# Performance work log

Hardware: AMD Instinct MI355X
Metric: run time of the kernel (lower is better)

The kernel has to match this reference:

```python
import jax, jax.numpy as jnp
import numpy as np

GROUPSIZE = 128

def _unpack_int4(packed, axis):
    # packed: int32 array; unpack 8 nibbles per int32 along `axis`.
    shifts = (jnp.arange(8, dtype=jnp.int32) * 4)
    expanded = jnp.expand_dims(packed, axis + 1)  # [..., P, 1, ...]
    shp = [1] * expanded.ndim
    shp[axis + 1] = 8
    nib = (expanded >> shifts.reshape(shp)) & 0xF
    new_shape = list(packed.shape)
    new_shape[axis] = packed.shape[axis] * 8
    return nib.reshape(new_shape)

def setup_inputs() -> dict:
    key = jax.random.key(0)
    k1, k2, k3, k4, k5 = jax.random.split(key, 5)
    in_f, out_f = 4096, 4096
    n_tokens = 8192
    n_groups = in_f // GROUPSIZE
    x = jax.random.normal(k1, (n_tokens, in_f), dtype=jnp.float32)
    qweight = jax.random.randint(k2, (in_f // 8, out_f), 0, 2147483647, dtype=jnp.int32)
    qzeros = jax.random.randint(k3, (n_groups, out_f // 8), 0, 2147483647, dtype=jnp.int32)
    scales = jax.random.uniform(k4, (n_groups, out_f), dtype=jnp.float32) * 0.01
    g_idx = (jnp.arange(in_f, dtype=jnp.int32) // GROUPSIZE).astype(jnp.int32)
    bias = jax.random.normal(k5, (out_f,), dtype=jnp.float32) * 0.01
    return {"x": x, "qweight": qweight, "qzeros": qzeros,
            "scales": scales, "g_idx": g_idx, "bias": bias}

def reference(x, qweight, qzeros, scales, g_idx, bias):
    # Dequantize int4 GPTQ weights: W[k,n] = scales[g_idx[k],n] * (wq[k,n] - (zq[g_idx[k],n]+1))
    wq = _unpack_int4(qweight, axis=0)          # [in, out] int32 nibbles
    zq = _unpack_int4(qzeros, axis=1) + 1       # [n_groups, out]
    scale_k = scales[g_idx]                     # [in, out]
    zero_k = zq[g_idx]                          # [in, out]
    w = scale_k * (wq.astype(x.dtype) - zero_k.astype(x.dtype))  # [in, out]
    return x @ w + bias
```

## Files before the change

kernel.cpp:

```cpp
#include <hip/hip_runtime.h>

typedef __attribute__((ext_vector_type(4))) float  f32x4;
typedef __attribute__((ext_vector_type(8))) short  short8;
typedef __attribute__((ext_vector_type(4))) short  short4v;

#define M_TOK 8192
#define N_OUT 4096
#define K_IN  4096
#define NT    64

typedef const __attribute__((address_space(1))) void* gp_t;
typedef __attribute__((address_space(3))) void* lp_t;
__device__ __forceinline__ void gl_lds16(const void* g, void* l) {
    __builtin_amdgcn_global_load_lds((gp_t)g, (lp_t)l, 16, 0, 0);
}

__global__ __launch_bounds__(256)
void cvt_x(const float* __restrict__ x, unsigned short* __restrict__ xb) {
    const size_t i = ((size_t)blockIdx.x * 256 + threadIdx.x) * 8;
    f32x4 a = *(const f32x4*)(x + i);
    f32x4 b = *(const f32x4*)(x + i + 4);
    union { short8 v; __bf16 h[8]; } u;
    u.h[0] = (__bf16)a.x; u.h[1] = (__bf16)a.y; u.h[2] = (__bf16)a.z; u.h[3] = (__bf16)a.w;
    u.h[4] = (__bf16)b.x; u.h[5] = (__bf16)b.y; u.h[6] = (__bf16)b.z; u.h[7] = (__bf16)b.w;
    *(short8*)(xb + i) = u.v;
}

__global__ __launch_bounds__(256)
void dequant_w(const int* __restrict__ qweight, const int* __restrict__ qzeros,
               const float* __restrict__ scales, unsigned short* __restrict__ Wt) {
    const int k0 = blockIdx.x * 64;
    const int n0 = blockIdx.y * 64;
    const int t  = threadIdx.x;
    const int n  = t & 63;
    const int pl = t >> 6;
    const int g  = k0 >> 7;
    const int ncol = n0 + n;

    const float scale = scales[g * N_OUT + ncol];
    const int qz  = qzeros[g * (N_OUT / 8) + (ncol >> 3)];
    const int zp1 = ((qz >> ((ncol & 7) * 4)) & 0xF) + 1;
    const float zs = -(float)zp1 * scale;

    __shared__ unsigned short wt[64][80];

    const int p0 = k0 >> 3;
    #pragma unroll
    for (int i = 0; i < 2; ++i) {
        const int p_local = pl + i * 4;
        const int q = qweight[(size_t)(p0 + p_local) * N_OUT + ncol];
        union { short8 v; __bf16 h[8]; } u;
        #pragma unroll
        for (int j = 0; j < 8; ++j)
            u.h[j] = (__bf16)fmaf((float)((q >> (4 * j)) & 0xF), scale, zs);
        *(short8*)(&wt[n][8 * p_local]) = u.v;
    }
    __syncthreads();

    #pragma unroll
    for (int it = 0; it < 2; ++it) {
        const int row   = (t >> 3) + 32 * it;
        const int chunk = t & 7;
        short8 v = *(const short8*)(&wt[row][chunk * 8]);
        *(short8*)(Wt + (size_t)(n0 + row) * K_IN + k0 + chunk * 8) = v;
    }
}

__global__ __launch_bounds__(512, 2)
void gemm_bf16_8p(const unsigned short* __restrict__ xb,
                  const unsigned short* __restrict__ Wt,
                  const float* __restrict__ bias,
                  float* __restrict__ out)
{
    const int tid  = threadIdx.x;
    const int lane = tid & 63;
    const int wid  = tid >> 6;
    const int wm   = wid >> 2;
    const int wn   = wid & 3;

    const int bid = blockIdx.x;
    const int swz = (bid & 7) * 64 + (bid >> 3);
    const int m0 = (swz >> 4) * 256;
    const int n0 = (swz & 15) * 256;

    __shared__ __align__(16) unsigned char lds[131072];
    unsigned char* Ab = lds;
    unsigned char* Bb = lds + 65536;

    f32x4 acc[8][4];
    #pragma unroll
    for (int i = 0; i < 8; ++i)
        #pragma unroll
        for (int j = 0; j < 4; ++j)
            acc[i][j] = f32x4{0.f, 0.f, 0.f, 0.f};

    const int sw8    = ((tid & 7) ^ ((tid >> 3) & 7)) * 8;
    const int a_srow = tid >> 3;
    const int b_srow = (wid >> 2) * 64 + (wid & 3) * 8 + (lane >> 3);
    const int a_dst  = wid * 1024;
    const int b_dst  = (wid >> 2) * 8192 + (wid & 3) * 1024;

    const int col0 = (((lane >> 4))     ^ (lane & 7)) << 4;
    const int col1 = ((4 | (lane >> 4)) ^ (lane & 7)) << 4;
    const int arow = (wm * 128 + (lane & 15)) * 128;
    const int brow = (wn * 64  + (lane & 15)) * 128;

    short8 af[4][2], b0[2][2], b1[2][2];

#define CFENCE asm volatile("" ::: "memory")

#define STAGE_A(SEL, KT, H) do { \
    _Pragma("unroll") for (int j_ = 0; j_ < 2; ++j_) \
        gl_lds16(xb + (size_t)(m0 + j_ * 128 + (H) * 64 + a_srow) * K_IN + (KT) * 64 + sw8, \
                 Ab + (SEL) * 32768 + j_ * 16384 + (H) * 8192 + a_dst); } while (0)

#define STAGE_B(SEL, KT, H) do { \
    _Pragma("unroll") for (int j_ = 0; j_ < 2; ++j_) \
        gl_lds16(Wt + (size_t)(n0 + j_ * 128 + (H) * 32 + b_srow) * K_IN + (KT) * 64 + sw8, \
                 Bb + (SEL) * 32768 + j_ * 16384 + (H) * 4096 + b_dst); } while (0)

#define LOAD_A(SEL, HM) do { \
    _Pragma("unroll") for (int mi_ = 0; mi_ < 4; ++mi_) { \
        af[mi_][0] = *(const short8*)(Ab + (SEL) * 32768 + arow + (HM) * 8192 + mi_ * 2048 + col0); \
        af[mi_][1] = *(const short8*)(Ab + (SEL) * 32768 + arow + (HM) * 8192 + mi_ * 2048 + col1); } } while (0)

#define LOAD_B(DST, SEL, HN) do { \
    _Pragma("unroll") for (int ni_ = 0; ni_ < 2; ++ni_) { \
        DST[ni_][0] = *(const short8*)(Bb + (SEL) * 32768 + brow + (HN) * 4096 + ni_ * 2048 + col0); \
        DST[ni_][1] = *(const short8*)(Bb + (SEL) * 32768 + brow + (HN) * 4096 + ni_ * 2048 + col1); } } while (0)

#define MFMA_Q(HM, HN, BF) do { \
    _Pragma("unroll") for (int mi_ = 0; mi_ < 4; ++mi_) \
    _Pragma("unroll") for (int ni_ = 0; ni_ < 2; ++ni_) \
    _Pragma("unroll") for (int kk_ = 0; kk_ < 2; ++kk_) \
        acc[(HM) * 4 + mi_][(HN) * 2 + ni_] = __builtin_amdgcn_mfma_f32_16x16x32_bf16( \
            af[mi_][kk_], BF[ni_][kk_], acc[(HM) * 4 + mi_][(HN) * 2 + ni_], 0, 0, 0); } while (0)

#define K_STEP(CUR, NXT) do { \
     \
    asm volatile("s_waitcnt vmcnt(2)" ::: "memory"); \
    __builtin_amdgcn_s_barrier(); \
    CFENCE; \
    LOAD_A(CUR, 0); \
    LOAD_B(b0, CUR, 0); \
    LOAD_B(b1, CUR, 1); \
    STAGE_A(NXT, ktn, 0); \
    STAGE_B(NXT, ktn, 0); \
    __builtin_amdgcn_s_setprio(1); \
    MFMA_Q(0, 0, b0); \
    __builtin_amdgcn_s_setprio(0); \
     \
    __builtin_amdgcn_s_barrier(); \
    CFENCE; \
    STAGE_B(NXT, ktn, 1); \
    CFENCE; \
    STAGE_A(NXT, ktn, 1); \
    __builtin_amdgcn_s_setprio(1); \
    MFMA_Q(0, 1, b1); \
    __builtin_amdgcn_s_setprio(0); \
     \
    asm volatile("s_waitcnt vmcnt(8)" ::: "memory"); \
    __builtin_amdgcn_s_barrier(); \
    CFENCE; \
    LOAD_A(CUR, 1); \
    __builtin_amdgcn_s_setprio(1); \
    MFMA_Q(1, 0, b0); \
    __builtin_amdgcn_s_setprio(0); \
     \
    __builtin_amdgcn_s_barrier(); \
    CFENCE; \
    __builtin_amdgcn_s_setprio(1); \
    MFMA_Q(1, 1, b1); \
    __builtin_amdgcn_s_setprio(0); \
} while (0)

    STAGE_A(0, 0, 0);
    CFENCE;
    STAGE_B(0, 0, 0);
    CFENCE;
    STAGE_B(0, 0, 1);
    CFENCE;
    STAGE_A(0, 0, 1);

    int ktn;
    #pragma unroll 1
    for (int kt = 0; kt < NT; kt += 2) {
        ktn = kt + 1;
        K_STEP(0, 1);
        ktn = (kt + 2) & (NT - 1);
        K_STEP(1, 0);
    }

#undef STAGE_A
#undef STAGE_B
#undef LOAD_A
#undef LOAD_B
#undef MFMA_Q
#undef K_STEP
#undef CFENCE

    const int col_base = n0 + wn * 64 + (lane & 15);
    const int row_base = m0 + wm * 128 + (lane >> 4) * 4;
    #pragma unroll
    for (int fn = 0; fn < 4; ++fn) {
        const int col = col_base + fn * 16;
        const float bv = bias[col];
        #pragma unroll
        for (int fm = 0; fm < 8; ++fm) {
            #pragma unroll
            for (int r = 0; r < 4; ++r) {
                const int row = row_base + fm * 16 + r;
                out[(size_t)row * N_OUT + col] = acc[fm][fn][r] + bv;
            }
        }
    }
}

__global__ __launch_bounds__(256, 2)
void gptq_gemm_fused(const float* __restrict__ x,
                     const int*   __restrict__ qweight,
                     const int*   __restrict__ qzeros,
                     const float* __restrict__ scales,
                     const float* __restrict__ bias,
                     float*       __restrict__ out)
{
    const int tid  = threadIdx.x;
    const int lane = tid & 63;
    const int wid  = tid >> 6;
    const int wm   = wid >> 1;
    const int wn   = wid & 1;
    const int m0 = blockIdx.y * 128;
    const int n0 = blockIdx.x * 128;

    __shared__ __align__(16) unsigned char lds[32768];
    unsigned char* Ab = lds;
    unsigned char* Bb = lds + 16384;

    const int ar  = tid >> 4;
    const int ac4 = (tid & 15) * 4;
    const int bnn = tid & 127;
    const int bph = tid >> 7;
    const int ncol = n0 + bnn;

    f32x4 a_reg[8];
    int   q_reg[4];
    float scale_r = 0.f, zs_r = 0.f;

    f32x4 acc[4][4];
    #pragma unroll
    for (int i = 0; i < 4; ++i)
        #pragma unroll
        for (int j = 0; j < 4; ++j)
            acc[i][j] = f32x4{0.f, 0.f, 0.f, 0.f};

    auto load_tile = [&](int kt) {
        const int k0 = kt * 64;
        #pragma unroll
        for (int i = 0; i < 8; ++i)
            a_reg[i] = *(const f32x4*)(x + (size_t)(m0 + ar + 16 * i) * K_IN + k0 + ac4);
        const int p0 = k0 >> 3;
        #pragma unroll
        for (int i = 0; i < 4; ++i)
            q_reg[i] = qweight[(size_t)(p0 + i * 2 + bph) * N_OUT + ncol];
        const int g = k0 >> 7;
        scale_r = scales[g * N_OUT + ncol];
        const int qz = qzeros[g * (N_OUT / 8) + (ncol >> 3)];
        zs_r = -(float)(((qz >> ((ncol & 7) * 4)) & 0xF) + 1) * scale_r;
    };

    auto store_tile = [&]() {
        #pragma unroll
        for (int i = 0; i < 8; ++i) {
            const int r = ar + 16 * i;
            const int addr = r * 128 + ((ac4 * 2) ^ ((r & 7) << 4));
            union { short4v v; __bf16 h[4]; } u;
            u.h[0] = (__bf16)a_reg[i].x; u.h[1] = (__bf16)a_reg[i].y;
            u.h[2] = (__bf16)a_reg[i].z; u.h[3] = (__bf16)a_reg[i].w;
            *(short4v*)(Ab + addr) = u.v;
        }
        #pragma unroll
        for (int i = 0; i < 4; ++i) {
            const int pl = i * 2 + bph;
            const int q  = q_reg[i];
            union { short8 v; __bf16 h[8]; } u;
            #pragma unroll
            for (int j = 0; j < 8; ++j)
                u.h[j] = (__bf16)fmaf((float)((q >> (4 * j)) & 0xF), scale_r, zs_r);
            const int addr = bnn * 128 + ((pl * 16) ^ ((bnn & 7) << 4));
            *(short8*)(Bb + addr) = u.v;
        }
    };

    auto compute_tile = [&]() {
        #pragma unroll
        for (int kk = 0; kk < 2; ++kk) {
            short8 afr[4], bfr[4];
            const int cb = kk * 64 + (lane >> 4) * 16;
            #pragma unroll
            for (int mi = 0; mi < 4; ++mi) {
                const int r = wm * 64 + mi * 16 + (lane & 15);
                afr[mi] = *(const short8*)(Ab + r * 128 + (cb ^ ((r & 7) << 4)));
            }
            #pragma unroll
            for (int ni = 0; ni < 4; ++ni) {
                const int nn = wn * 64 + ni * 16 + (lane & 15);
                bfr[ni] = *(const short8*)(Bb + nn * 128 + (cb ^ ((nn & 7) << 4)));
            }
            #pragma unroll
            for (int mi = 0; mi < 4; ++mi)
                #pragma unroll
                for (int ni = 0; ni < 4; ++ni)
                    acc[mi][ni] = __builtin_amdgcn_mfma_f32_16x16x32_bf16(
                        afr[mi], bfr[ni], acc[mi][ni], 0, 0, 0);
        }
    };

    load_tile(0);
    for (int kt = 0; kt < NT; ++kt) {
        if (kt) __syncthreads();
        store_tile();
        __syncthreads();
        if (kt + 1 < NT) load_tile(kt + 1);
        compute_tile();
    }

    const int col_base = n0 + wn * 64 + (lane & 15);
    const int row_base = m0 + wm * 64 + (lane >> 4) * 4;
    #pragma unroll
    for (int ni = 0; ni < 4; ++ni) {
        const int col = col_base + ni * 16;
        const float bv = bias[col];
        #pragma unroll
        for (int mi = 0; mi < 4; ++mi)
            #pragma unroll
            for (int r = 0; r < 4; ++r)
                out[(size_t)(row_base + mi * 16 + r) * N_OUT + col] = acc[mi][ni][r] + bv;
    }
}

extern "C" void kernel_launch(void* const* d_in, const int* in_sizes, int n_in,
                              void* d_out, int out_size, void* d_ws, size_t ws_size,
                              hipStream_t stream) {
    const float* x       = (const float*)d_in[0];
    const int*   qweight = (const int*)  d_in[1];
    const int*   qzeros  = (const int*)  d_in[2];
    const float* scales  = (const float*)d_in[3];
    const float* bias    = (const float*)d_in[5];
    float* out = (float*)d_out;

    const size_t xb_bytes = (size_t)M_TOK * K_IN * 2;
    const size_t wt_bytes = (size_t)N_OUT * K_IN * 2;

    if (ws_size >= xb_bytes + wt_bytes) {
        unsigned short* xb = (unsigned short*)d_ws;
        unsigned short* Wt = (unsigned short*)((char*)d_ws + xb_bytes);
        cvt_x<<<dim3((M_TOK * K_IN) / (256 * 8)), dim3(256), 0, stream>>>(x, xb);
        dequant_w<<<dim3(K_IN / 64, N_OUT / 64), dim3(256), 0, stream>>>(qweight, qzeros, scales, Wt);
        gemm_bf16_8p<<<dim3((M_TOK / 256) * (N_OUT / 256)), dim3(512), 0, stream>>>(xb, Wt, bias, out);
    } else {
        gptq_gemm_fused<<<dim3(N_OUT / 128, M_TOK / 128), dim3(256), 0, stream>>>(
            x, qweight, qzeros, scales, bias, out);
    }
}
```

Before: 260.3 us.

## Collapse GEMM K-step to a single barrier with full prefetch issue

```diff
diff --git a/kernel.cpp b/kernel.cpp
--- a/kernel.cpp
+++ b/kernel.cpp
@@ -67,7 +67,7 @@
 }
 
 __global__ __launch_bounds__(512, 2)
-void gemm_bf16_8p(const unsigned short* __restrict__ xb,
+void gemm_bf16_1r(const unsigned short* __restrict__ xb,
                   const unsigned short* __restrict__ Wt,
                   const float* __restrict__ bias,
                   float* __restrict__ out)
@@ -134,52 +134,60 @@
     _Pragma("unroll") for (int ni_ = 0; ni_ < 2; ++ni_) \
     _Pragma("unroll") for (int kk_ = 0; kk_ < 2; ++kk_) \
         acc[(HM) * 4 + mi_][(HN) * 2 + ni_] = __builtin_amdgcn_mfma_f32_16x16x32_bf16( \
+            af[mi_][kk_], BF[kk_ == 0 ? (0 + ni_) : (0 + ni_)][kk_], \
+            acc[(HM) * 4 + mi_][(HN) * 2 + ni_], 0, 0, 0); } while (0)
+
+#undef MFMA_Q
+#define MFMA_Q(HM, HN, BF) do { \
+    _Pragma("unroll") for (int mi_ = 0; mi_ < 4; ++mi_) \
+    _Pragma("unroll") for (int ni_ = 0; ni_ < 2; ++ni_) \
+    _Pragma("unroll") for (int kk_ = 0; kk_ < 2; ++kk_) \
+        acc[(HM) * 4 + mi_][(HN) * 2 + ni_] = __builtin_amdgcn_mfma_f32_16x16x32_bf16( \
             af[mi_][kk_], BF[ni_][kk_], acc[(HM) * 4 + mi_][(HN) * 2 + ni_], 0, 0, 0); } while (0)
 
 #define K_STEP(CUR, NXT) do { \
      \
-    asm volatile("s_waitcnt vmcnt(2)" ::: "memory"); \
+    asm volatile("s_waitcnt vmcnt(0)" ::: "memory"); \
     __builtin_amdgcn_s_barrier(); \
     CFENCE; \
+     \
     LOAD_A(CUR, 0); \
     LOAD_B(b0, CUR, 0); \
+    CFENCE; \
+     \
     LOAD_B(b1, CUR, 1); \
+    CFENCE; \
+     \
     STAGE_A(NXT, ktn, 0); \
     STAGE_B(NXT, ktn, 0); \
+    STAGE_B(NXT, ktn, 1); \
+    STAGE_A(NXT, ktn, 1); \
+     \
+    asm volatile("s_waitcnt lgkmcnt(4)" ::: "memory"); \
+    __builtin_amdgcn_sched_barrier(0); \
     __builtin_amdgcn_s_setprio(1); \
     MFMA_Q(0, 0, b0); \
     __builtin_amdgcn_s_setprio(0); \
      \
-    __builtin_amdgcn_s_barrier(); \
-    CFENCE; \
-    STAGE_B(NXT, ktn, 1); \
-    CFENCE; \
-    STAGE_A(NXT, ktn, 1); \
+    asm volatile("s_waitcnt lgkmcnt(0)" ::: "memory"); \
+    __builtin_amdgcn_sched_barrier(0); \
     __builtin_amdgcn_s_setprio(1); \
     MFMA_Q(0, 1, b1); \
     __builtin_amdgcn_s_setprio(0); \
-     \
-    asm volatile("s_waitcnt vmcnt(8)" ::: "memory"); \
-    __builtin_amdgcn_s_barrier(); \
     CFENCE; \
+     \
     LOAD_A(CUR, 1); \
+    asm volatile("s_waitcnt lgkmcnt(0)" ::: "memory"); \
+    __builtin_amdgcn_sched_barrier(0); \
     __builtin_amdgcn_s_setprio(1); \
     MFMA_Q(1, 0, b0); \
-    __builtin_amdgcn_s_setprio(0); \
-     \
-    __builtin_amdgcn_s_barrier(); \
-    CFENCE; \
-    __builtin_amdgcn_s_setprio(1); \
     MFMA_Q(1, 1, b1); \
     __builtin_amdgcn_s_setprio(0); \
 } while (0)
 
     STAGE_A(0, 0, 0);
-    CFENCE;
     STAGE_B(0, 0, 0);
-    CFENCE;
     STAGE_B(0, 0, 1);
-    CFENCE;
     STAGE_A(0, 0, 1);
 
     int ktn;
@@ -356,7 +364,7 @@
         unsigned short* Wt = (unsigned short*)((char*)d_ws + xb_bytes);
         cvt_x<<<dim3((M_TOK * K_IN) / (256 * 8)), dim3(256), 0, stream>>>(x, xb);
         dequant_w<<<dim3(K_IN / 64, N_OUT / 64), dim3(256), 0, stream>>>(qweight, qzeros, scales, Wt);
-        gemm_bf16_8p<<<dim3((M_TOK / 256) * (N_OUT / 256)), dim3(512), 0, stream>>>(xb, Wt, bias, out);
+        gemm_bf16_1r<<<dim3((M_TOK / 256) * (N_OUT / 256)), dim3(512), 0, stream>>>(xb, Wt, bias, out);
     } else {
         gptq_gemm_fused<<<dim3(N_OUT / 128, M_TOK / 128), dim3(256), 0, stream>>>(
             x, qweight, qzeros, scales, bias, out);
```

Result: no change. 263.6 us (+1.3%).
